# Kernel tuning notes

Hardware: AMD Instinct MI355X
Metric: run time of the kernel (lower is better)

Reference implementation:

```python
import jax, jax.numpy as jnp
import numpy as np

SIGMA = 3.0
LW = 12            # int(4*sigma + 0.5)
HIGH = 0.2
LOW = 0.1
THRES = 0.0
EPS = 1e-9
GAMMA = 0.005
H = W = 28


def _corr1d_zero(x, k):
    # cross-correlation along last axis with zero padding (torch Conv1d semantics)
    lw = (k.shape[0] - 1) // 2
    xp = jnp.pad(x, [(0, 0)] * (x.ndim - 1) + [(lw, lw)])
    n = x.shape[-1]
    out = k[0] * xp[..., 0:n]
    for i in range(1, k.shape[0]):
        out = out + k[i] * xp[..., i:i + n]
    return out


def _gaussian2d(x, k):
    # module smooths along H first (after transpose), then along W, zero padding
    y = jnp.swapaxes(_corr1d_zero(jnp.swapaxes(x, 2, 3), k), 2, 3)
    return _corr1d_zero(y, k)


def _deriv_last(x):
    # [-1,0,1] cross-correlation with replicate padding
    xp = jnp.pad(x, [(0, 0)] * (x.ndim - 1) + [(1, 1)], mode='edge')
    return xp[..., 2:] - xp[..., :-2]


def _smooth_last(x):
    # [1,2,1] with replicate padding
    xp = jnp.pad(x, [(0, 0)] * (x.ndim - 1) + [(1, 1)], mode='edge')
    return xp[..., :-2] + 2.0 * xp[..., 1:-1] + xp[..., 2:]


def _nb(a, dr, dc):
    # value of a at (r+dr, c+dc), zero outside (borders are masked by erosion anyway)
    p = jnp.pad(a, ((0, 0), (0, 0), (1, 1), (1, 1)))
    return p[:, :, 1 + dr:1 + dr + H, 1 + dc:1 + dc + W]


def _sector(pts, m, w, c1p, c2p, c1m, c2m, bug):
    ip = c2p * w + c1p * (1.0 - w)
    im = c2m * w + c1m * (1.0 - w)
    s1 = jax.nn.relu(GAMMA - m + ip)
    # faithful to original: the 90-135 sector reuses the 'plus' interpolation for s2
    s2 = jax.nn.relu(GAMMA - m + (ip if bug else im))
    s = jnp.where(pts, jnp.maximum(s1, s2), 0.0)
    return s, (ip <= m) & (im <= m)


def _dilate(b):
    p = jnp.pad(b, 1)
    out = jnp.zeros_like(b)
    for dr in (-1, 0, 1):
        for dc in (-1, 0, 1):
            out = out | p[1 + dr:1 + dr + H, 1 + dc:1 + dc + W]
    return out


def _forward(x, mask, gauss_kernel):
    bleed = _gaussian2d(mask, gauss_kernel)
    xs = _gaussian2d(x, gauss_kernel) / (bleed + 1e-12)

    # jsobel: derivative along W, smoothing along H; isobel: derivative along H, smoothing along W
    jsob = jnp.swapaxes(_smooth_last(jnp.swapaxes(_deriv_last(xs), 2, 3)), 2, 3)
    isob = _smooth_last(jnp.swapaxes(_deriv_last(jnp.swapaxes(xs, 2, 3)), 2, 3))

    ai = jnp.abs(isob)
    aj = jnp.abs(jsob)
    mag2 = isob * isob + jsob * jsob
    mag = jnp.sqrt(mag2 + EPS)
    mag = mag * (mag > THRES).astype(mag.dtype)

    # binary erosion of mask with full 3x3 structure, border_value=0
    mb = mask[0, 0] != 0
    mp = jnp.pad(mb, 1)
    er2 = jnp.ones((H, W), bool)
    for dr in (-1, 0, 1):
        for dc in (-1, 0, 1):
            er2 = er2 & mp[1 + dr:1 + dr + H, 1 + dc:1 + dc + W]
    er = (er2 & (mag2[0, 0] > 0))[None, None]

    same = ((isob >= 0) & (jsob >= 0)) | ((isob <= 0) & (jsob <= 0))
    opp = ((isob <= 0) & (jsob >= 0)) | ((isob >= 0) & (jsob <= 0))

    nb = lambda dr, dc: _nb(mag, dr, dc)
    m = mag

    # 0-45 degrees
    pts0 = er & same & (ai >= aj)
    w0 = aj / (ai + EPS)
    s0, l0 = _sector(pts0, m, w0, nb(1, 0), nb(1, 1), nb(-1, 0), nb(-1, -1), False)
    # 45-90 degrees
    pts1 = er & same & (ai <= aj)
    w1 = ai / jnp.where(pts1, aj, 1.0)
    s1, l1 = _sector(pts1, m, w1, nb(0, 1), nb(1, 1), nb(0, -1), nb(-1, -1), False)
    # 90-135 degrees (replicates original s2-uses-plus-interp quirk)
    pts2 = er & opp & (ai <= aj)
    w2 = ai / jnp.where(pts2, aj, 1.0)
    s2, l2 = _sector(pts2, m, w2, nb(0, 1), nb(-1, 1), nb(0, -1), nb(1, -1), True)
    # 135-180 degrees
    pts3 = er & opp & (ai >= aj)
    w3 = aj / jnp.where(pts3, ai, 1.0)
    s3, l3 = _sector(pts3, m, w3, nb(-1, 0), nb(-1, 1), nb(1, 0), nb(1, -1), False)

    # sequential overwrite like torch local_maxima[pts] = ...
    lm = jnp.zeros(mag.shape, bool)
    for p, l in ((pts0, l0), (pts1, l1), (pts2, l2), (pts3, l3)):
        lm = jnp.where(p, l, lm)

    # hysteresis: keep low-threshold pixels 8-connected to a high-threshold pixel
    lm2 = lm[0, 0]
    mg = mag[0, 0]
    high = lm2 & (mg >= HIGH)
    low = lm2 & (mg >= LOW)
    final = jax.lax.fori_loop(0, 2 * H, lambda i, c: _dilate(c) & low, high)
    mask_final = final.astype(mag.dtype)[None, None]

    mag_out = jax.lax.stop_gradient(mask_final) + mag - jax.lax.stop_gradient(mag)
    test = jnp.ones_like(mag)
    return (s0, s1, s2, s3, lm, test, mag_out)


def setup_inputs():
    key = jax.random.key(0)
    x = jax.random.uniform(key, (1, 1, H, W), dtype=jnp.float32)
    mask = jnp.ones((1, 1, H, W), jnp.float32)
    t = np.arange(-LW, LW + 1).astype(np.float64)
    g = np.exp(-0.5 * t * t / (SIGMA * SIGMA))
    g = (g / g.sum()).astype(np.float32)
    return {"x": x, "mask": mask, "gauss_kernel": jnp.asarray(g)}


def reference(x, mask, gauss_kernel):
    return _forward(x, mask, gauss_kernel)
```

## Files before the change

kernel.cpp:

```cpp
#include <hip/hip_runtime.h>

#define HH 28
#define WW 28
#define NPIX 784
#define LWD 12
#define KLEN 25
#define PH (HH + 2 * LWD)
#define PW (WW + 2 * LWD)
#define NPAD (PH * WW)
#define NT 832

__global__ __launch_bounds__(NT) void canny_all(
    const float* __restrict__ x, const float* __restrict__ mask,
    const float* __restrict__ g, float* __restrict__ out)
{
    __shared__ float spx[NPAD], spm[NPAD];
    __shared__ float t1x[NPAD], t1m[NPAD];
    __shared__ float sxs[NPIX], smag[NPIX];
    __shared__ unsigned rowHigh[HH], rowLow[HH], rowFinal[HH];
    __shared__ float sg[KLEN];

    const int tid = threadIdx.x;
    if (tid < KLEN) sg[tid] = g[tid];
    if (tid < HH) { rowHigh[tid] = 0u; rowLow[tid] = 0u; }

    for (int j = tid; j < NPAD; j += NT) {
        const int pr = j / WW;
        const int pc = j - pr * WW;
        float vx = 0.0f, vm = 0.0f;
        if (pr >= LWD && pr < LWD + HH) {
            vx = x[(pr - LWD) * WW + pc];
            vm = mask[(pr - LWD) * WW + pc];
        }
        spx[j] = vx; spm[j] = vm;
        const int c2 = j % PW;
        if (c2 < LWD || c2 >= LWD + WW) { t1x[j] = 0.0f; t1m[j] = 0.0f; }
    }
    __syncthreads();

    const int r = tid / WW, c = tid - (tid / WW) * WW;

    if (tid < NPIX) {
        float ax = 0.0f, am = 0.0f;
        #pragma unroll
        for (int i = 0; i < KLEN; ++i) {
            const float gv = sg[i];
            ax += gv * spx[tid + i * WW];
            am += gv * spm[tid + i * WW];
        }
        t1x[r * PW + c + LWD] = ax;
        t1m[r * PW + c + LWD] = am;
    }
    __syncthreads();

    if (tid < NPIX) {
        float ax = 0.0f, am = 0.0f;
        const int base = r * PW + c;
        #pragma unroll
        for (int i = 0; i < KLEN; ++i) {
            const float gv = sg[i];
            ax += gv * t1x[base + i];
            am += gv * t1m[base + i];
        }
        sxs[tid] = ax / (am + 1e-12f);
    }
    __syncthreads();

    float isob = 0.0f, jsob = 0.0f, m = 0.0f, ai = 0.0f, aj = 0.0f;
    bool er = false;
    if (tid < NPIX) {
        const int rm = (r > 0) ? r - 1 : 0, rp = (r < HH - 1) ? r + 1 : r;
        const int cm = (c > 0) ? c - 1 : 0, cp = (c < WW - 1) ? c + 1 : c;
        const float x_mm = sxs[rm * WW + cm], x_m0 = sxs[rm * WW + c], x_mp = sxs[rm * WW + cp];
        const float x_0m = sxs[r  * WW + cm],                          x_0p = sxs[r  * WW + cp];
        const float x_pm = sxs[rp * WW + cm], x_p0 = sxs[rp * WW + c], x_pp = sxs[rp * WW + cp];
        const float dU = x_mp - x_mm, dC = x_0p - x_0m, dD = x_pp - x_pm;
        jsob = (dU + 2.0f * dC) + dD;
        const float hL = x_pm - x_mm, hC = x_p0 - x_m0, hR = x_pp - x_mp;
        isob = (hL + 2.0f * hC) + hR;

        const float mag2 = isob * isob + jsob * jsob;
        m = sqrtf(mag2 + 1e-9f);
        smag[tid] = m;
        ai = fabsf(isob); aj = fabsf(jsob);

        bool er2 = (r >= 1) && (r <= HH - 2) && (c >= 1) && (c <= WW - 2);
        if (er2) {
            #pragma unroll
            for (int dr = -1; dr <= 1; ++dr)
                #pragma unroll
                for (int dc = -1; dc <= 1; ++dc)
                    er2 = er2 && (spm[(r + dr + LWD) * WW + (c + dc)] != 0.0f);
        }
        er = er2 && (mag2 > 0.0f);
    }
    __syncthreads();

    if (tid < NPIX) {
        const bool same = ((isob >= 0.0f) && (jsob >= 0.0f)) || ((isob <= 0.0f) && (jsob <= 0.0f));
        const bool opp  = ((isob <= 0.0f) && (jsob >= 0.0f)) || ((isob >= 0.0f) && (jsob <= 0.0f));
        const float GAMMA = 0.005f;
        float s0v = 0.0f, s1v = 0.0f, s2v = 0.0f, s3v = 0.0f;
        bool lmv = false;

        #define NB(dr, dc) (smag[(r + (dr)) * WW + (c + (dc))])

        if (er && same && (ai >= aj)) {
            const float w  = aj / (ai + 1e-9f);
            const float ip = NB(1, 1)   * w + NB(1, 0)   * (1.0f - w);
            const float im = NB(-1, -1) * w + NB(-1, 0)  * (1.0f - w);
            const float a = fmaxf(GAMMA - m + ip, 0.0f);
            const float b = fmaxf(GAMMA - m + im, 0.0f);
            s0v = fmaxf(a, b);
            lmv = (ip <= m) && (im <= m);
        }
        if (er && same && (ai <= aj)) {
            const float w  = ai / aj;
            const float ip = NB(1, 1)   * w + NB(0, 1)  * (1.0f - w);
            const float im = NB(-1, -1) * w + NB(0, -1) * (1.0f - w);
            const float a = fmaxf(GAMMA - m + ip, 0.0f);
            const float b = fmaxf(GAMMA - m + im, 0.0f);
            s1v = fmaxf(a, b);
            lmv = (ip <= m) && (im <= m);
        }
        if (er && opp && (ai <= aj)) {
            const float w  = ai / aj;
            const float ip = NB(-1, 1) * w + NB(0, 1)  * (1.0f - w);
            const float im = NB(1, -1) * w + NB(0, -1) * (1.0f - w);
            const float a = fmaxf(GAMMA - m + ip, 0.0f);
            s2v = a;
            lmv = (ip <= m) && (im <= m);
        }
        if (er && opp && (ai >= aj)) {
            const float w  = aj / ai;
            const float ip = NB(-1, 1) * w + NB(-1, 0) * (1.0f - w);
            const float im = NB(1, -1) * w + NB(1, 0)  * (1.0f - w);
            const float a = fmaxf(GAMMA - m + ip, 0.0f);
            const float b = fmaxf(GAMMA - m + im, 0.0f);
            s3v = fmaxf(a, b);
            lmv = (ip <= m) && (im <= m);
        }
        #undef NB

        out[0 * NPIX + tid] = s0v;
        out[1 * NPIX + tid] = s1v;
        out[2 * NPIX + tid] = s2v;
        out[3 * NPIX + tid] = s3v;
        out[4 * NPIX + tid] = lmv ? 1.0f : 0.0f;
        out[5 * NPIX + tid] = 1.0f;

        if (lmv && (m >= 0.2f)) atomicOr(&rowHigh[r], 1u << c);
        if (lmv && (m >= 0.1f)) atomicOr(&rowLow[r],  1u << c);
    }
    __syncthreads();

    if (tid < 64) {
        unsigned cur = 0u, lo = 0u;
        if (tid < HH) { cur = rowHigh[tid]; lo = rowLow[tid]; }
        for (int it = 0; it < 2 * HH; ++it) {
            const unsigned up = __shfl(cur, (tid + 63) & 63, 64);
            const unsigned dn = __shfl(cur, (tid + 1)  & 63, 64);
            const unsigned mg = up | cur | dn;
            const unsigned nxt = (mg | (mg << 1) | (mg >> 1)) & lo;
            const bool chg = (nxt != cur);
            cur = nxt;
            if (!__any((int)chg)) break;
        }
        if (tid < HH) rowFinal[tid] = cur;
    }
    __syncthreads();

    if (tid < NPIX) {
        out[6 * NPIX + tid] = (float)((rowFinal[r] >> c) & 1u);
    }
}

extern "C" void kernel_launch(void* const* d_in, const int* in_sizes, int n_in,
                              void* d_out, int out_size, void* d_ws, size_t ws_size,
                              hipStream_t stream) {
    const float* x    = (const float*)d_in[0];
    const float* mask = (const float*)d_in[1];
    const float* g    = (const float*)d_in[2];
    float* out = (float*)d_out;
    canny_all<<<1, NT, 0, stream>>>(x, mask, g, out);
}
```

Measured before the change: 61.05 us.

## Interleave image and mask into float2 shared buffers and write final mask directly

```diff
diff --git a/kernel.cpp b/kernel.cpp
--- a/kernel.cpp
+++ b/kernel.cpp
@@ -14,10 +14,10 @@
     const float* __restrict__ x, const float* __restrict__ mask,
     const float* __restrict__ g, float* __restrict__ out)
 {
-    __shared__ float spx[NPAD], spm[NPAD];
-    __shared__ float t1x[NPAD], t1m[NPAD];
+    __shared__ float2 sp[NPAD];
+    __shared__ float2 t1[NPAD];
     __shared__ float sxs[NPIX], smag[NPIX];
-    __shared__ unsigned rowHigh[HH], rowLow[HH], rowFinal[HH];
+    __shared__ unsigned rowHigh[HH], rowLow[HH];
     __shared__ float sg[KLEN];
 
     const int tid = threadIdx.x;
@@ -32,9 +32,9 @@
             vx = x[(pr - LWD) * WW + pc];
             vm = mask[(pr - LWD) * WW + pc];
         }
-        spx[j] = vx; spm[j] = vm;
+        sp[j] = make_float2(vx, vm);
         const int c2 = j % PW;
-        if (c2 < LWD || c2 >= LWD + WW) { t1x[j] = 0.0f; t1m[j] = 0.0f; }
+        if (c2 < LWD || c2 >= LWD + WW) t1[j] = make_float2(0.0f, 0.0f);
     }
     __syncthreads();
 
@@ -45,11 +45,11 @@
         #pragma unroll
         for (int i = 0; i < KLEN; ++i) {
             const float gv = sg[i];
-            ax += gv * spx[tid + i * WW];
-            am += gv * spm[tid + i * WW];
+            const float2 t = sp[tid + i * WW];
+            ax = fmaf(gv, t.x, ax);
+            am = fmaf(gv, t.y, am);
         }
-        t1x[r * PW + c + LWD] = ax;
-        t1m[r * PW + c + LWD] = am;
+        t1[r * PW + c + LWD] = make_float2(ax, am);
     }
     __syncthreads();
 
@@ -59,8 +59,9 @@
         #pragma unroll
         for (int i = 0; i < KLEN; ++i) {
             const float gv = sg[i];
-            ax += gv * t1x[base + i];
-            am += gv * t1m[base + i];
+            const float2 t = t1[base + i];
+            ax = fmaf(gv, t.x, ax);
+            am = fmaf(gv, t.y, am);
         }
         sxs[tid] = ax / (am + 1e-12f);
     }
@@ -90,7 +91,7 @@
             for (int dr = -1; dr <= 1; ++dr)
                 #pragma unroll
                 for (int dc = -1; dc <= 1; ++dc)
-                    er2 = er2 && (spm[(r + dr + LWD) * WW + (c + dc)] != 0.0f);
+                    er2 = er2 && (sp[(r + dr + LWD) * WW + (c + dc)].y != 0.0f);
         }
         er = er2 && (mag2 > 0.0f);
     }
@@ -166,12 +167,16 @@
             cur = nxt;
             if (!__any((int)chg)) break;
         }
-        if (tid < HH) rowFinal[tid] = cur;
-    }
-    __syncthreads();
-
-    if (tid < NPIX) {
-        out[6 * NPIX + tid] = (float)((rowFinal[r] >> c) & 1u);
+        if (tid < HH) {
+            float4* op = (float4*)(out + 6 * NPIX + tid * WW);
+            #pragma unroll
+            for (int q = 0; q < 7; ++q) {
+                op[q] = make_float4((float)((cur >> (4 * q + 0)) & 1u),
+                                    (float)((cur >> (4 * q + 1)) & 1u),
+                                    (float)((cur >> (4 * q + 2)) & 1u),
+                                    (float)((cur >> (4 * q + 3)) & 1u));
+            }
+        }
     }
 }
 
```

Result: faster. 59.81 us (-2.0%).
